# Kernel optimization log

Measured on AMD Instinct MI355X. Metric: run time of the kernel, lower is better.

## Reference

```python
import jax, jax.numpy as jnp
import numpy as np

T, N, E = 64, 10000, 160000
NIN, NHID, NOUT = 64, 128, 64

def _xavier(key, shape):
    # xavier_normal_ for Linear/GCNConv lin weights of shape [out, in]
    std = jnp.sqrt(2.0 / (shape[0] + shape[1])).astype(jnp.float32)
    return std * jax.random.normal(key, shape, dtype=jnp.float32)

def setup_inputs() -> dict:
    key = jax.random.key(0)
    ks = jax.random.split(key, 12)
    x = jax.random.normal(ks[0], (T, N, NIN), dtype=jnp.float32)
    src = jax.random.randint(ks[1], (E,), 0, N)
    dst = jax.random.randint(ks[2], (E,), 0, N)
    edge_index = jnp.stack([src, dst])  # [2, E], PyG convention src->dst
    m_in = dst   # receiver index per edge (one-hot row of incidence matrix)
    m_out = src  # sender index per edge
    b = 0.1 * jnp.ones((NHID,), jnp.float32)
    return {
        "x": x, "edge_index": edge_index, "m_in": m_in, "m_out": m_out,
        "Wi": _xavier(ks[3], (NHID, NIN + NHID)), "bi": b,
        "Wf": _xavier(ks[4], (NHID, NIN + NHID)), "bf": b,
        "Wo": _xavier(ks[5], (NHID, NIN + NHID)), "bo": b,
        "Wg": _xavier(ks[6], (NHID, NIN + NHID)), "bg": b,
        "W1": _xavier(ks[7], (NHID, 2 * NHID)), "b1": b,
        "Wc": _xavier(ks[8], (NOUT, NHID)), "bc": 0.1 * jnp.ones((NOUT,), jnp.float32),
    }

def reference(x, edge_index, m_in, m_out, Wi, bi, Wf, bf, Wo, bo, Wg, bg, W1, b1, Wc, bc):
    n = x.shape[1]
    src, dst = edge_index[0], edge_index[1]
    loop = jnp.arange(n)
    s = jnp.concatenate([src, loop])  # self-loops appended (GCNConv default)
    d = jnp.concatenate([dst, loop])
    deg = jax.ops.segment_sum(jnp.ones_like(d, x.dtype), d, num_segments=n)
    dinv = jnp.where(deg > 0, deg, 1.0) ** -0.5  # deg>=1 with self-loops
    norm = (dinv[s] * dinv[d])[:, None]

    def gcn(z, W, b):
        zw = z @ W.T                    # [n, out]
        return jax.ops.segment_sum(zw[s] * norm, d, num_segments=n) + b

    def step(carry, xt):
        h, c = carry
        comb = jnp.concatenate([xt, h], axis=-1)  # [n, n_in+n_hid]
        i = jax.nn.sigmoid(gcn(comb, Wi, bi))
        f = jax.nn.sigmoid(gcn(comb, Wf, bf))
        o = jax.nn.sigmoid(gcn(comb, Wo, bo))
        g = jnp.tanh(gcn(comb, Wg, bg))
        c = f * c + i * g
        h = o * jnp.tanh(c)
        return (h, c), None

    h0 = jnp.zeros((n, NHID), x.dtype)
    (h, _), _ = jax.lax.scan(step, (h0, h0), x)

    # node2edge: concat receiver and sender hidden states  [E, 2*n_hid]
    e = jnp.concatenate([h[m_in], h[m_out]], axis=-1)
    e = jax.nn.relu(e @ W1.T + b1)  # dropout p=0.0 -> identity
    # edge2node: scatter-sum edge features to receiver nodes
    nodes = jax.ops.segment_sum(e, m_in, num_segments=n)
    return gcn(nodes, Wc, bc)
```

## Files before the change

### kernel.cpp

```cpp
#include <hip/hip_runtime.h>
#include <math.h>

#define NIN 64
#define NHID 128
#define NOUT 64

typedef __bf16 bf16x8 __attribute__((ext_vector_type(8)));
typedef float  floatx4 __attribute__((ext_vector_type(4)));

__device__ __forceinline__ float sigmoidf(float x){ return 1.0f/(1.0f+expf(-x)); }
__device__ __forceinline__ float b2f_lo(unsigned p){ unsigned b = p<<16; return __uint_as_float(b); }
__device__ __forceinline__ float b2f_hi(unsigned p){ unsigned b = p & 0xffff0000u; return __uint_as_float(b); }
__device__ __forceinline__ unsigned f2pk(float lo, float hi){
  __bf16 a=(__bf16)lo, b=(__bf16)hi;
  unsigned short ua, ub;
  __builtin_memcpy(&ua,&a,2); __builtin_memcpy(&ub,&b,2);
  return (unsigned)ua | ((unsigned)ub<<16);
}

__global__ void k_deg_init(int* __restrict__ deg, int n){
  int v = blockIdx.x*256 + threadIdx.x;
  if(v<n) deg[v] = 1;
}
__global__ void k_deg_count(const int* __restrict__ dst, int E, int* __restrict__ deg){
  int e = blockIdx.x*256 + threadIdx.x;
  if(e<E) atomicAdd(&deg[dst[e]], 1);
}
__global__ void k_dinv(const int* __restrict__ deg, float* __restrict__ dinv, int n){
  int v = blockIdx.x*256 + threadIdx.x;
  if(v<n) dinv[v] = rsqrtf((float)deg[v]);
}
__global__ __launch_bounds__(1024) void k_scan(const int* __restrict__ deg,
    int* __restrict__ row_ptr, int* __restrict__ fill, int n){
  __shared__ int lds[1024];
  __shared__ int s_carry;
  if(threadIdx.x==0) s_carry=0;
  __syncthreads();
  int nchunk=(n+1023)/1024;
  for(int ch=0; ch<nchunk; ++ch){
    int v = ch*1024 + threadIdx.x;
    int val = (v<n)? (deg[v]-1) : 0;
    lds[threadIdx.x]=val;
    __syncthreads();
    for(int off=1; off<1024; off<<=1){
      int t=(threadIdx.x>=off)? lds[threadIdx.x-off] : 0;
      __syncthreads();
      lds[threadIdx.x]+=t;
      __syncthreads();
    }
    int incl=lds[threadIdx.x];
    int carry=s_carry;
    if(v<n){ row_ptr[v]=carry+incl-val; fill[v]=carry+incl-val; }
    __syncthreads();
    if(threadIdx.x==1023) s_carry=carry+lds[1023];
    __syncthreads();
  }
  if(threadIdx.x==0) row_ptr[n]=s_carry;
}
__global__ void k_fill(const int* __restrict__ src, const int* __restrict__ dst, int E,
                       int* __restrict__ fill, int* __restrict__ ecol){
  int e = blockIdx.x*256 + threadIdx.x;
  if(e<E){
    int d = dst[e];
    int pos = atomicAdd(&fill[d], 1);
    ecol[pos] = src[e];
  }
}

__global__ void k_prep_wb(const float* __restrict__ Wi, const float* __restrict__ Wf,
                          const float* __restrict__ Wo, const float* __restrict__ Wg,
                          __bf16* __restrict__ Wb){
  int idx = blockIdx.x*256 + threadIdx.x;
  if(idx >= 32*6*64*8) return;
  int jj = idx & 7;
  int L  = (idx >> 3) & 63;
  int t  = idx >> 9;
  int kt = t - (t/6)*6, CT = t/6;
  int colj = CT*16 + (L & 15);
  int k    = kt*32 + ((L >> 4) << 3) + jj;
  int gate = colj >> 7, jg = colj & 127;
  const float* W = (gate==0)? Wi : (gate==1)? Wf : (gate==2)? Wo : Wg;
  Wb[idx] = (__bf16)W[jg*192 + k];
}
__global__ void k_prep_w1(const float* __restrict__ W1, float* __restrict__ W1t){
  int idx = blockIdx.x*256 + threadIdx.x;
  if(idx >= 128*256) return;
  int k = idx >> 8, j = idx & 255;
  W1t[idx] = (j<128)? W1[j*256+k] : W1[(j-128)*256+128+k];
}
__global__ void k_prep_wc(const float* __restrict__ Wc, float* __restrict__ Wct){
  int idx = blockIdx.x*256 + threadIdx.x;
  if(idx >= 128*64) return;
  int k = idx/64, j = idx%64;
  Wct[idx] = Wc[j*128+k];
}

__global__ void k_init(unsigned* __restrict__ hpA, unsigned* __restrict__ hpB,
                       float* __restrict__ cbuf, __bf16* __restrict__ xs,
                       int NP, int T){
  int i = blockIdx.x*256 + threadIdx.x;
  if(i < (NP+1)*64){ hpA[i]=0u; hpB[i]=0u; }
  if(i < NP*128) cbuf[i]=0.f;
  if(i < T*64){ int t=i>>6, f=i&63; xs[((size_t)t*(NP+1) + NP)*64 + f] = (__bf16)0.f; }
}

__global__ void k_xscale(const float* __restrict__ x, const float* __restrict__ dinv,
                         __bf16* __restrict__ xs, int n, int NP){
  int i = blockIdx.x*256 + threadIdx.x;
  if(i >= n*64) return;
  int t = blockIdx.y;
  xs[((size_t)t*(NP+1))*64 + i] = (__bf16)(x[(size_t)t*(size_t)n*64 + i]*dinv[i>>6]);
}

__global__ __launch_bounds__(512,5) void k_step(
    const __bf16* __restrict__ xst,
    const unsigned* __restrict__ hp_prev,
    unsigned* __restrict__ hp_cur,
    float* __restrict__ cbuf,
    float* __restrict__ hbuf,
    const int* __restrict__ row_ptr, const int* __restrict__ ecol,
    const float* __restrict__ dinv, const __bf16* __restrict__ Wb,
    const float* __restrict__ bi, const float* __restrict__ bf_,
    const float* __restrict__ bo, const float* __restrict__ bg,
    int n, int NP, int last)
{
  __shared__ __align__(16) __bf16 s_a[6*544];
  __shared__ int   s_col[1024];
  __shared__ int   s_deg[16];
  __shared__ int   s_beg[16];
  __shared__ float s_dv[16];
  const int tid=threadIdx.x, wv=tid>>6, l=tid&63;
  const int l15=l&15, quad=l>>4;
  const int v0=blockIdx.x*16;

  if(tid<16){
    int v=v0+tid;
    int beg=(v<n)? row_ptr[v]:0, end=(v<n)? row_ptr[v+1]:0;
    s_beg[tid]=beg; s_deg[tid]=end-beg;
    s_dv[tid]=(v<n)? dinv[v]:0.f;
  }
  __syncthreads();
  for(int idx=tid; idx<1024; idx+=512){
    int m=idx>>6, kk=idx&63;
    s_col[idx]=(kk<s_deg[m])? ecol[s_beg[m]+kk] : NP;
  }
  __syncthreads();

  float ax[2], alo[2], ahi[2];
  int K;
  {
    int d0=s_deg[2*wv], d1=s_deg[2*wv+1];
    d0=d0>64?64:d0; d1=d1>64?64:d1;
    K=d0>d1?d0:d1;
  }
  #pragma unroll
  for(int i=0;i<2;++i){
    int v=v0+2*wv+i;
    ax[i]=(float)xst[(size_t)v*64+l];
    unsigned p=hp_prev[(size_t)v*64+l];
    alo[i]=b2f_lo(p); ahi[i]=b2f_hi(p);
  }
  const int* cr=&s_col[(2*wv)*64];
  #pragma unroll 2
  for(int kk=0;kk<K;++kk){
    int u0=cr[kk], u1=cr[64+kk];
    float    x0=(float)xst[(size_t)u0*64+l];
    unsigned p0=hp_prev[(size_t)u0*64+l];
    float    x1=(float)xst[(size_t)u1*64+l];
    unsigned p1=hp_prev[(size_t)u1*64+l];
    ax[0]+=x0; alo[0]+=b2f_lo(p0); ahi[0]+=b2f_hi(p0);
    ax[1]+=x1; alo[1]+=b2f_lo(p1); ahi[1]+=b2f_hi(p1);
  }
  #pragma unroll
  for(int i=0;i<2;++i){
    int m=2*wv+i, d=s_deg[m];
    if(d>64){
      for(int e2=s_beg[m]+64;e2<s_beg[m]+d;++e2){
        int u=ecol[e2];
        ax[i]+=(float)xst[(size_t)u*64+l];
        unsigned p=hp_prev[(size_t)u*64+l];
        alo[i]+=b2f_lo(p); ahi[i]+=b2f_hi(p);
      }
    }
  }
  {
    int kt0=l>>5, q0=(l>>3)&3, j0=l&7;
    int L2=2*l, kt1=2+(L2>>5), q1=(L2>>3)&3, j1=L2&7;
    #pragma unroll
    for(int i=0;i<2;++i){
      int m=2*wv+i; float dv=s_dv[m];
      s_a[kt0*544+q0*136+m*8+j0]=(__bf16)(dv*ax[i]);
      *(__shared__ unsigned*)&s_a[kt1*544+q1*136+m*8+j1]=f2pk(dv*alo[i],dv*ahi[i]);
    }
  }
  __syncthreads();

  bf16x8 af[6];
  #pragma unroll
  for(int kt=0;kt<6;++kt)
    af[kt]=*(__shared__ bf16x8*)&s_a[kt*544+quad*136+l15*8];
  const int jg=16*wv+l15;
  floatx4 acc[4];
  {
    const float* bs0=bi; const float* bs1=bf_; const float* bs2=bo; const float* bs3=bg;
    #pragma unroll
    for(int g=0;g<4;++g){
      const float* bsel = (g==0)? bs0 : (g==1)? bs1 : (g==2)? bs2 : bs3;
      float b=bsel[jg];
      floatx4 a={b,b,b,b};
      const __bf16* bp=Wb + (size_t)((8*g+wv)*6)*512 + (size_t)l*8;
      #pragma unroll
      for(int kt=0;kt<6;++kt)
        a=__builtin_amdgcn_mfma_f32_16x16x32_bf16(af[kt],*(const bf16x8*)(bp+kt*512),a,0,0,0);
      acc[g]=a;
    }
  }

  #pragma unroll
  for(int r=0;r<4;++r){
    int m=quad*4+r, v=v0+m;
    float I=sigmoidf(acc[0][r]);
    float F=sigmoidf(acc[1][r]);
    float O=sigmoidf(acc[2][r]);
    float G=tanhf  (acc[3][r]);
    size_t coff=(size_t)v*128+jg;
    float cn=F*cbuf[coff]+I*G;
    cbuf[coff]=cn;
    float hn=O*tanhf(cn);
    float hs=s_dv[m]*hn;
    float hs2=__shfl_xor(hs,1,64);
    if((l15&1)==0)
      hp_cur[(size_t)v*64+(jg>>1)]=f2pk(hs,hs2);
    if(last) hbuf[coff]=hn;
  }
}

__global__ __launch_bounds__(256) void k_head1(const float* __restrict__ h,
    const float* __restrict__ W1t, float* __restrict__ Hio, int n){
  __shared__ float s_h[16][NHID];
  int v0 = blockIdx.x*16;
  for(int i=threadIdx.x; i<16*NHID; i+=256){
    int m = i/NHID, k = i - m*NHID;
    int v = v0 + m;
    s_h[m][k] = (v<n)? h[(size_t)v*NHID + k] : 0.0f;
  }
  __syncthreads();
  int j = threadIdx.x;
  float acc[16];
  #pragma unroll
  for(int m=0;m<16;++m) acc[m]=0.f;
  for(int k=0;k<NHID;++k){
    float w = W1t[k*256 + j];
    #pragma unroll
    for(int m=0;m<16;++m) acc[m] = fmaf(w, s_h[m][k], acc[m]);
  }
  for(int m=0;m<16;++m){
    int v = v0 + m;
    if(v >= n) break;
    Hio[(size_t)v*256 + j] = acc[m];
  }
}
__global__ __launch_bounds__(256) void k_e2n(const float* __restrict__ Hio,
    const int* __restrict__ row_ptr, const int* __restrict__ col,
    const float* __restrict__ b1, float* __restrict__ nodes, int n){
  int wv = threadIdx.x >> 6, lane = threadIdx.x & 63;
  int v = blockIdx.x*4 + wv;
  if(v >= n) return;
  float base0 = Hio[(size_t)v*256 + lane]      + b1[lane];
  float base1 = Hio[(size_t)v*256 + 64 + lane] + b1[64+lane];
  float a0=0.f, a1=0.f;
  int beg=row_ptr[v], end=row_ptr[v+1];
  for(int e=beg; e<end; ++e){
    int u = col[e];
    float t0 = base0 + Hio[(size_t)u*256 + 128 + lane];
    float t1 = base1 + Hio[(size_t)u*256 + 192 + lane];
    a0 += fmaxf(t0, 0.0f);
    a1 += fmaxf(t1, 0.0f);
  }
  nodes[(size_t)v*NHID + lane]      = a0;
  nodes[(size_t)v*NHID + 64 + lane] = a1;
}
__global__ __launch_bounds__(64) void k_head2(const float* __restrict__ nodes,
    const float* __restrict__ Wct, float* __restrict__ tmp, int n){
  __shared__ float s_n[16][NHID];
  int v0 = blockIdx.x*16;
  for(int i=threadIdx.x; i<16*NHID; i+=64){
    int m = i/NHID, k = i - m*NHID;
    int v = v0 + m;
    s_n[m][k] = (v<n)? nodes[(size_t)v*NHID + k] : 0.0f;
  }
  __syncthreads();
  int j = threadIdx.x;
  float acc[16];
  #pragma unroll
  for(int m=0;m<16;++m) acc[m]=0.f;
  for(int k=0;k<NHID;++k){
    float w = Wct[k*64 + j];
    #pragma unroll
    for(int m=0;m<16;++m) acc[m] = fmaf(w, s_n[m][k], acc[m]);
  }
  for(int m=0;m<16;++m){
    int v = v0 + m;
    if(v >= n) break;
    tmp[(size_t)v*64 + j] = acc[m];
  }
}
__global__ __launch_bounds__(256) void k_final(const float* __restrict__ tmp,
    const int* __restrict__ row_ptr, const int* __restrict__ col,
    const float* __restrict__ dinv, const float* __restrict__ bc,
    float* __restrict__ out, int n){
  int wv = threadIdx.x >> 6, lane = threadIdx.x & 63;
  int v = blockIdx.x*4 + wv;
  if(v >= n) return;
  float dv = dinv[v];
  float acc = dv*dv*tmp[(size_t)v*64 + lane];
  int beg=row_ptr[v], end=row_ptr[v+1];
  for(int e=beg; e<end; ++e){
    int u = col[e];
    acc = fmaf(dv*dinv[u], tmp[(size_t)u*64 + lane], acc);
  }
  out[(size_t)v*64 + lane] = acc + bc[lane];
}

extern "C" void kernel_launch(void* const* d_in, const int* in_sizes, int n_in,
                              void* d_out, int out_size, void* d_ws, size_t ws_size,
                              hipStream_t stream) {
  (void)n_in; (void)ws_size;
  const float* x  = (const float*)d_in[0];
  const int*   ei = (const int*)d_in[1];
  const float* Wi = (const float*)d_in[4];  const float* bi  = (const float*)d_in[5];
  const float* Wf = (const float*)d_in[6];  const float* bf_ = (const float*)d_in[7];
  const float* Wo = (const float*)d_in[8];  const float* bo  = (const float*)d_in[9];
  const float* Wg = (const float*)d_in[10]; const float* bg  = (const float*)d_in[11];
  const float* W1 = (const float*)d_in[12]; const float* b1  = (const float*)d_in[13];
  const float* Wc = (const float*)d_in[14]; const float* bc  = (const float*)d_in[15];
  float* out = (float*)d_out;

  const int E = in_sizes[2];
  const int n = out_size / NOUT;
  const int T = in_sizes[0] / (n * NIN);
  const int ntiles = (n + 15)/16;
  const int NP = ntiles*16;
  const int* srcl = ei;
  const int* dstl = ei + E;

  char* p = (char*)d_ws;
  auto alloc = [&](size_t bytes){ char* r = p; p += ((bytes + 255)/256)*256; return r; };
  int*      deg     = (int*)     alloc((size_t)n*4);
  float*    dinv    = (float*)   alloc((size_t)n*4);
  int*      row_ptr = (int*)     alloc((size_t)(n+1)*4);
  int*      fill    = (int*)     alloc((size_t)n*4);
  int*      ecol    = (int*)     alloc((size_t)E*4);
  __bf16*   Wb      = (__bf16*)  alloc((size_t)32*6*64*8*2);
  float*    W1t     = (float*)   alloc((size_t)128*256*4);
  float*    Wct     = (float*)   alloc((size_t)128*64*4);
  __bf16*   xs      = (__bf16*)  alloc((size_t)T*(NP+1)*64*2);
  unsigned* hpA     = (unsigned*)alloc((size_t)(NP+1)*64*4);
  unsigned* hpB     = (unsigned*)alloc((size_t)(NP+1)*64*4);
  float*    cbuf    = (float*)   alloc((size_t)NP*128*4);
  float*    hbuf    = (float*)   alloc((size_t)NP*128*4);
  float*    Hio     = (float*)   alloc((size_t)NP*256*4);
  float*    nodes   = (float*)   alloc((size_t)n*NHID*4);
  float*    tmp     = (float*)   alloc((size_t)NP*64*4);

  int gn = (n+255)/256;
  int gE = (E+255)/256;

  k_deg_init <<<gn, 256, 0, stream>>>(deg, n);
  k_deg_count<<<gE, 256, 0, stream>>>(dstl, E, deg);
  k_dinv     <<<gn, 256, 0, stream>>>(deg, dinv, n);
  k_scan     <<<1, 1024, 0, stream>>>(deg, row_ptr, fill, n);
  k_fill     <<<gE, 256, 0, stream>>>(srcl, dstl, E, fill, ecol);

  k_prep_wb<<<(32*6*64*8+255)/256, 256, 0, stream>>>(Wi, Wf, Wo, Wg, Wb);
  k_prep_w1<<<(128*256+255)/256, 256, 0, stream>>>(W1, W1t);
  k_prep_wc<<<(128*64+255)/256, 256, 0, stream>>>(Wc, Wct);

  k_init<<<((NP*128)+255)/256, 256, 0, stream>>>(hpA, hpB, cbuf, xs, NP, T);
  k_xscale<<<dim3((n*64+255)/256, T), 256, 0, stream>>>(x, dinv, xs, n, NP);

  for(int t=0; t<T; ++t){
    const __bf16* xst = xs + (size_t)t*(size_t)(NP+1)*64;
    const unsigned* hp = (t & 1)? hpB : hpA;
    unsigned*       hc = (t & 1)? hpA : hpB;
    k_step<<<ntiles, 512, 0, stream>>>(xst, hp, hc, cbuf, hbuf, row_ptr, ecol, dinv,
                                       Wb, bi, bf_, bo, bg, n, NP, (t==T-1)?1:0);
  }

  k_head1<<<ntiles, 256, 0, stream>>>(hbuf, W1t, Hio, n);
  k_e2n  <<<(n+3)/4, 256, 0, stream>>>(Hio, row_ptr, ecol, b1, nodes, n);
  k_head2<<<(n+15)/16, 64, 0, stream>>>(nodes, Wct, tmp, n);
  k_final<<<(n+3)/4, 256, 0, stream>>>(tmp, row_ptr, ecol, dinv, bc, out, n);
}
```

Measured before the change: 1.630 ms.

## Halve k_step block size with four nodes per wave, vectorize xscale, unroll gathers

```diff
diff --git a/kernel.cpp b/kernel.cpp
--- a/kernel.cpp
+++ b/kernel.cpp
@@ -107,12 +107,18 @@
 __global__ void k_xscale(const float* __restrict__ x, const float* __restrict__ dinv,
                          __bf16* __restrict__ xs, int n, int NP){
   int i = blockIdx.x*256 + threadIdx.x;
-  if(i >= n*64) return;
+  if(i >= n*8) return;
   int t = blockIdx.y;
-  xs[((size_t)t*(NP+1))*64 + i] = (__bf16)(x[(size_t)t*(size_t)n*64 + i]*dinv[i>>6]);
-}
-
-__global__ __launch_bounds__(512,5) void k_step(
+  float dv = dinv[i>>3];
+  const float4* xp = (const float4*)(x + (size_t)t*(size_t)n*64) + (size_t)i*2;
+  float4 a = xp[0], b = xp[1];
+  bf16x8 o;
+  o[0]=(__bf16)(a.x*dv); o[1]=(__bf16)(a.y*dv); o[2]=(__bf16)(a.z*dv); o[3]=(__bf16)(a.w*dv);
+  o[4]=(__bf16)(b.x*dv); o[5]=(__bf16)(b.y*dv); o[6]=(__bf16)(b.z*dv); o[7]=(__bf16)(b.w*dv);
+  *(bf16x8*)(xs + ((size_t)t*(NP+1))*64 + (size_t)i*8) = o;
+}
+
+__global__ __launch_bounds__(256,4) void k_step(
     const __bf16* __restrict__ xst,
     const unsigned* __restrict__ hp_prev,
     unsigned* __restrict__ hp_cur,
@@ -140,40 +146,43 @@
     s_dv[tid]=(v<n)? dinv[v]:0.f;
   }
   __syncthreads();
-  for(int idx=tid; idx<1024; idx+=512){
+  for(int idx=tid; idx<1024; idx+=256){
     int m=idx>>6, kk=idx&63;
     s_col[idx]=(kk<s_deg[m])? ecol[s_beg[m]+kk] : NP;
   }
   __syncthreads();
 
-  float ax[2], alo[2], ahi[2];
+  float ax[4], alo[4], ahi[4];
   int K;
   {
-    int d0=s_deg[2*wv], d1=s_deg[2*wv+1];
-    d0=d0>64?64:d0; d1=d1>64?64:d1;
-    K=d0>d1?d0:d1;
-  }
-  #pragma unroll
-  for(int i=0;i<2;++i){
-    int v=v0+2*wv+i;
+    int d0=s_deg[4*wv+0]; d0=d0>64?64:d0;
+    int d1=s_deg[4*wv+1]; d1=d1>64?64:d1;
+    int d2=s_deg[4*wv+2]; d2=d2>64?64:d2;
+    int d3=s_deg[4*wv+3]; d3=d3>64?64:d3;
+    int m01=d0>d1?d0:d1, m23=d2>d3?d2:d3;
+    K=m01>m23?m01:m23;
+  }
+  #pragma unroll
+  for(int i=0;i<4;++i){
+    int v=v0+4*wv+i;
     ax[i]=(float)xst[(size_t)v*64+l];
     unsigned p=hp_prev[(size_t)v*64+l];
     alo[i]=b2f_lo(p); ahi[i]=b2f_hi(p);
   }
-  const int* cr=&s_col[(2*wv)*64];
+  const int* cr=&s_col[(4*wv)*64];
   #pragma unroll 2
   for(int kk=0;kk<K;++kk){
-    int u0=cr[kk], u1=cr[64+kk];
-    float    x0=(float)xst[(size_t)u0*64+l];
-    unsigned p0=hp_prev[(size_t)u0*64+l];
-    float    x1=(float)xst[(size_t)u1*64+l];
-    unsigned p1=hp_prev[(size_t)u1*64+l];
-    ax[0]+=x0; alo[0]+=b2f_lo(p0); ahi[0]+=b2f_hi(p0);
-    ax[1]+=x1; alo[1]+=b2f_lo(p1); ahi[1]+=b2f_hi(p1);
-  }
-  #pragma unroll
-  for(int i=0;i<2;++i){
-    int m=2*wv+i, d=s_deg[m];
+    #pragma unroll
+    for(int i=0;i<4;++i){
+      int u=cr[i*64+kk];
+      float xv=(float)xst[(size_t)u*64+l];
+      unsigned p=hp_prev[(size_t)u*64+l];
+      ax[i]+=xv; alo[i]+=b2f_lo(p); ahi[i]+=b2f_hi(p);
+    }
+  }
+  #pragma unroll
+  for(int i=0;i<4;++i){
+    int m=4*wv+i, d=s_deg[m];
     if(d>64){
       for(int e2=s_beg[m]+64;e2<s_beg[m]+d;++e2){
         int u=ecol[e2];
@@ -187,8 +196,8 @@
     int kt0=l>>5, q0=(l>>3)&3, j0=l&7;
     int L2=2*l, kt1=2+(L2>>5), q1=(L2>>3)&3, j1=L2&7;
     #pragma unroll
-    for(int i=0;i<2;++i){
-      int m=2*wv+i; float dv=s_dv[m];
+    for(int i=0;i<4;++i){
+      int m=4*wv+i; float dv=s_dv[m];
       s_a[kt0*544+q0*136+m*8+j0]=(__bf16)(dv*ax[i]);
       *(__shared__ unsigned*)&s_a[kt1*544+q1*136+m*8+j1]=f2pk(dv*alo[i],dv*ahi[i]);
     }
@@ -199,39 +208,40 @@
   #pragma unroll
   for(int kt=0;kt<6;++kt)
     af[kt]=*(__shared__ bf16x8*)&s_a[kt*544+quad*136+l15*8];
-  const int jg=16*wv+l15;
-  floatx4 acc[4];
-  {
-    const float* bs0=bi; const float* bs1=bf_; const float* bs2=bo; const float* bs3=bg;
+
+  #pragma unroll
+  for(int h2=0;h2<2;++h2){
+    const int ct=2*wv+h2;
+    const int jg=16*ct+l15;
+    floatx4 acc[4];
     #pragma unroll
     for(int g=0;g<4;++g){
-      const float* bsel = (g==0)? bs0 : (g==1)? bs1 : (g==2)? bs2 : bs3;
+      const float* bsel = (g==0)? bi : (g==1)? bf_ : (g==2)? bo : bg;
       float b=bsel[jg];
       floatx4 a={b,b,b,b};
-      const __bf16* bp=Wb + (size_t)((8*g+wv)*6)*512 + (size_t)l*8;
+      const __bf16* bp=Wb + (size_t)((8*g+ct)*6)*512 + (size_t)l*8;
       #pragma unroll
       for(int kt=0;kt<6;++kt)
         a=__builtin_amdgcn_mfma_f32_16x16x32_bf16(af[kt],*(const bf16x8*)(bp+kt*512),a,0,0,0);
       acc[g]=a;
     }
-  }
-
-  #pragma unroll
-  for(int r=0;r<4;++r){
-    int m=quad*4+r, v=v0+m;
-    float I=sigmoidf(acc[0][r]);
-    float F=sigmoidf(acc[1][r]);
-    float O=sigmoidf(acc[2][r]);
-    float G=tanhf  (acc[3][r]);
-    size_t coff=(size_t)v*128+jg;
-    float cn=F*cbuf[coff]+I*G;
-    cbuf[coff]=cn;
-    float hn=O*tanhf(cn);
-    float hs=s_dv[m]*hn;
-    float hs2=__shfl_xor(hs,1,64);
-    if((l15&1)==0)
-      hp_cur[(size_t)v*64+(jg>>1)]=f2pk(hs,hs2);
-    if(last) hbuf[coff]=hn;
+    #pragma unroll
+    for(int r=0;r<4;++r){
+      int m=quad*4+r, v=v0+m;
+      float I=sigmoidf(acc[0][r]);
+      float F=sigmoidf(acc[1][r]);
+      float O=sigmoidf(acc[2][r]);
+      float G=tanhf  (acc[3][r]);
+      size_t coff=(size_t)v*128+jg;
+      float cn=F*cbuf[coff]+I*G;
+      cbuf[coff]=cn;
+      float hn=O*tanhf(cn);
+      float hs=s_dv[m]*hn;
+      float hs2=__shfl_xor(hs,1,64);
+      if((l15&1)==0)
+        hp_cur[(size_t)v*64+(jg>>1)]=f2pk(hs,hs2);
+      if(last) hbuf[coff]=hn;
+    }
   }
 }
 
@@ -270,12 +280,20 @@
   float base1 = Hio[(size_t)v*256 + 64 + lane] + b1[64+lane];
   float a0=0.f, a1=0.f;
   int beg=row_ptr[v], end=row_ptr[v+1];
-  for(int e=beg; e<end; ++e){
+  int e=beg;
+  for(; e+1<end; e+=2){
+    int u0 = col[e], u1 = col[e+1];
+    float p0 = Hio[(size_t)u0*256 + 128 + lane];
+    float q0 = Hio[(size_t)u0*256 + 192 + lane];
+    float p1 = Hio[(size_t)u1*256 + 128 + lane];
+    float q1 = Hio[(size_t)u1*256 + 192 + lane];
+    a0 += fmaxf(base0 + p0, 0.0f) + fmaxf(base0 + p1, 0.0f);
+    a1 += fmaxf(base1 + q0, 0.0f) + fmaxf(base1 + q1, 0.0f);
+  }
+  if(e<end){
     int u = col[e];
-    float t0 = base0 + Hio[(size_t)u*256 + 128 + lane];
-    float t1 = base1 + Hio[(size_t)u*256 + 192 + lane];
-    a0 += fmaxf(t0, 0.0f);
-    a1 += fmaxf(t1, 0.0f);
+    a0 += fmaxf(base0 + Hio[(size_t)u*256 + 128 + lane], 0.0f);
+    a1 += fmaxf(base1 + Hio[(size_t)u*256 + 192 + lane], 0.0f);
   }
   nodes[(size_t)v*NHID + lane]      = a0;
   nodes[(size_t)v*NHID + 64 + lane] = a1;
@@ -315,7 +333,16 @@
   float dv = dinv[v];
   float acc = dv*dv*tmp[(size_t)v*64 + lane];
   int beg=row_ptr[v], end=row_ptr[v+1];
-  for(int e=beg; e<end; ++e){
+  int e=beg;
+  for(; e+1<end; e+=2){
+    int u0 = col[e], u1 = col[e+1];
+    float d0 = dinv[u0], d1 = dinv[u1];
+    float t0 = tmp[(size_t)u0*64 + lane];
+    float t1 = tmp[(size_t)u1*64 + lane];
+    acc = fmaf(dv*d0, t0, acc);
+    acc = fmaf(dv*d1, t1, acc);
+  }
+  if(e<end){
     int u = col[e];
     acc = fmaf(dv*dinv[u], tmp[(size_t)u*64 + lane], acc);
   }
@@ -377,13 +404,13 @@
   k_prep_wc<<<(128*64+255)/256, 256, 0, stream>>>(Wc, Wct);
 
   k_init<<<((NP*128)+255)/256, 256, 0, stream>>>(hpA, hpB, cbuf, xs, NP, T);
-  k_xscale<<<dim3((n*64+255)/256, T), 256, 0, stream>>>(x, dinv, xs, n, NP);
+  k_xscale<<<dim3((n*8+255)/256, T), 256, 0, stream>>>(x, dinv, xs, n, NP);
 
   for(int t=0; t<T; ++t){
     const __bf16* xst = xs + (size_t)t*(size_t)(NP+1)*64;
     const unsigned* hp = (t & 1)? hpB : hpA;
     unsigned*       hc = (t & 1)? hpA : hpB;
-    k_step<<<ntiles, 512, 0, stream>>>(xst, hp, hc, cbuf, hbuf, row_ptr, ecol, dinv,
+    k_step<<<ntiles, 256, 0, stream>>>(xst, hp, hc, cbuf, hbuf, row_ptr, ecol, dinv,
                                        Wb, bi, bf_, bo, bg, n, NP, (t==T-1)?1:0);
   }
 
```

Measured after the change: 1.789 ms. 1.1x slower.
